# Performance work log

Hardware: AMD Instinct MI355X
Metric: run time of the kernel (lower is better)

## Reference

```python
import jax, jax.numpy as jnp
import numpy as np

IN_FEATURES = 8192
OUT_FEATURES = 28672
BATCH = 8  # tokens; skinny GEMM -> memory-bound weight streaming


def setup_inputs() -> dict:
    key = jax.random.key(0)
    k1, k2, k3, k4 = jax.random.split(key, 4)
    x = jax.random.normal(k1, (BATCH, IN_FEATURES), dtype=jnp.float32)
    # ternary codes in {0,1,2} -> weight values {-1,0,+1}; pack 4 codes / byte
    codes = jax.random.randint(k2, (OUT_FEATURES, IN_FEATURES), 0, 3, dtype=jnp.int32)
    codes4 = codes.reshape(OUT_FEATURES, IN_FEATURES // 4, 4)
    shifts = jnp.array([0, 2, 4, 6], dtype=jnp.int32)
    packed_weight = jnp.sum(codes4 << shifts, axis=-1).astype(jnp.int32)  # [O, I//4]
    weight_scale = jax.random.uniform(k3, (1,), dtype=jnp.float32, minval=0.01, maxval=0.1)
    bias = jax.random.normal(k4, (OUT_FEATURES,), dtype=jnp.float32)
    return {"x": x, "packed_weight": packed_weight, "weight_scale": weight_scale, "bias": bias}


def _unpack_ternary(packed):
    # [O, I//4] int -> [O, I] ternary in {-1,0,1}
    shifts = jnp.array([0, 2, 4, 6], dtype=jnp.int32)
    w = ((packed[:, :, None] >> shifts) & 3) - 1  # [O, I//4, 4]
    return w.reshape(packed.shape[0], -1)


def reference(x, packed_weight, weight_scale, bias):
    B = x.shape[0]
    x_flat = x.reshape(B, IN_FEATURES)
    # per-tensor absmax int8 activation quantization
    absmax = jnp.maximum(jnp.max(jnp.abs(x_flat)), 1e-5)
    act_scale = absmax / 127.0
    x_q = jnp.clip(jnp.round(x_flat / act_scale), -128, 127)  # int8 values, kept f32
    w = _unpack_ternary(packed_weight).astype(jnp.float32)  # [O, I]
    # fused dequant GEMM: integer-valued accumulation, single scalar scale
    acc = jnp.einsum('bi,oi->bo', x_q, w)  # exact in f32 (|acc| << 2^24)
    scale = weight_scale[0] * act_scale
    out = acc * scale + bias
    return out.reshape(B, OUT_FEATURES)
```

## Files before the change

### kernel.cpp

```cpp
#include <hip/hip_runtime.h>
#include <stdint.h>

#define O_FEATS 28672
#define I_FEATS 8192
#define BATCH 8
#define PITCH_W 260

typedef int i32x4 __attribute__((ext_vector_type(4)));


static __device__ __forceinline__ int unpack4(uint32_t p) {
  uint32_t lo = p & 0x0Fu;
  uint32_t hi = (p >> 4) & 0x0Fu;
  uint32_t a = (lo * 0x41u) & 0x0303u;
  uint32_t b = (hi * 0x41u) & 0x0303u;
  return (int)(a | (b << 16));
}

__global__ void k_absmax(const float* __restrict__ x, uint32_t* __restrict__ ws) {
  __shared__ float red[4];
  int t = threadIdx.x;
  float4 v = ((const float4*)x)[blockIdx.x * 256 + t];
  float m = fmaxf(fmaxf(fabsf(v.x), fabsf(v.y)), fmaxf(fabsf(v.z), fabsf(v.w)));
#pragma unroll
  for (int off = 32; off; off >>= 1)
    m = fmaxf(m, __shfl_xor(m, off));
  if ((t & 63) == 0) red[t >> 6] = m;
  __syncthreads();
  if (t == 0)
    ws[16 + blockIdx.x] =
        __float_as_uint(fmaxf(fmaxf(red[0], red[1]), fmaxf(red[2], red[3])));
}

__global__ void k_quant(const float* __restrict__ x, uint32_t* __restrict__ ws) {
  __shared__ float s_amax;
  __shared__ int reds[4];
  int t = threadIdx.x;
  if (blockIdx.x >= 64) {
    int row = 8 + ((blockIdx.x - 64) >> 3), seg = blockIdx.x & 7;
    int k0 = seg * 1024 + t * 4;
    int S = k0 >> 6, g = (k0 >> 4) & 3, j = k0 & 15;
    ws[1024 + ((S * 1024 + (g * 16 + row) * 16 + j) >> 2)] = 0u;
    return;
  }
  int b = blockIdx.x >> 3, seg = blockIdx.x & 7;
  if (t < 64) {
    float m = __uint_as_float(ws[16 + t]);
#pragma unroll
    for (int off = 32; off; off >>= 1)
      m = fmaxf(m, __shfl_xor(m, off));
    if (t == 0) {
      float a = fmaxf(m, 1e-5f);
      s_amax = a;
      ws[0] = __float_as_uint(a);
    }
  }
  __syncthreads();
  float s = s_amax / 127.0f;
  float4 v = ((const float4*)(x + b * I_FEATS + seg * 1024))[t];
  int q0 = (int)fminf(fmaxf(rintf(v.x / s), -128.f), 127.f);
  int q1 = (int)fminf(fmaxf(rintf(v.y / s), -128.f), 127.f);
  int q2 = (int)fminf(fmaxf(rintf(v.z / s), -128.f), 127.f);
  int q3 = (int)fminf(fmaxf(rintf(v.w / s), -128.f), 127.f);
  uint32_t pk = (uint32_t)(q0 & 0xff) | ((uint32_t)(q1 & 0xff) << 8) |
                ((uint32_t)(q2 & 0xff) << 16) | ((uint32_t)(q3 & 0xff) << 24);
  {
    int k0 = seg * 1024 + t * 4;
    int S = k0 >> 6, g = (k0 >> 4) & 3, j = k0 & 15;
    ws[1024 + ((S * 1024 + (g * 16 + b) * 16 + j) >> 2)] = pk;
  }
  int s4 = q0 + q1 + q2 + q3;
#pragma unroll
  for (int off = 32; off; off >>= 1)
    s4 += __shfl_xor(s4, off);
  if ((t & 63) == 0) reds[t >> 6] = s4;
  __syncthreads();
  if (t == 0)
    ws[128 + blockIdx.x] = (uint32_t)(reds[0] + reds[1] + reds[2] + reds[3]);
}

__global__ void __launch_bounds__(256, 4)
k_gemm(const int* __restrict__ Wp, const float* __restrict__ wscale,
       const float* __restrict__ bias, const uint32_t* __restrict__ ws,
       float* __restrict__ out) {
  __shared__ uint32_t Wlds[16 * PITCH_W];
  __shared__ int red[4][32][4];
  __shared__ int s_sumx[BATCH];
  __shared__ float s_scale;

  const int t = threadIdx.x;
  const int wave = t >> 6, lane = t & 63;

  if (t < 64) {
    int p = (int)ws[128 + t];
    p += __shfl_xor(p, 1);
    p += __shfl_xor(p, 2);
    p += __shfl_xor(p, 4);
    if ((t & 7) == 0) s_sumx[t >> 3] = p;
    if (t == 0) s_scale = (__uint_as_float(ws[0]) / 127.0f) * wscale[0];
  }

  const int o_base = blockIdx.x * 16;
  const int m = lane & 15, g = lane >> 4;

  const uint8_t* xqT = (const uint8_t*)(ws + 1024);
  const int4* ap = (const int4*)(xqT + (size_t)(wave * 4) * 1024 + lane * 16);

  const uint8_t* src_base =
      (const uint8_t*)Wp + (size_t)(o_base + wave * 4) * 8192 + lane * 16;
  uint32_t* lds_row0 = &Wlds[(wave * 4) * PITCH_W];

  const uint32_t* bp0 = &Wlds[m * PITCH_W + (wave * 256 + g * 16) / 4];

  i32x4 acc = {0, 0, 0, 0};

  for (int c = 0; c < 8; ++c) {
    __syncthreads();
#pragma unroll
    for (int i = 0; i < 4; ++i) {
      const uint32_t* src = (const uint32_t*)(src_base + (size_t)i * 8192 + c * 1024);
      __builtin_amdgcn_global_load_lds(src, lds_row0 + i * PITCH_W, 16, 0, 0);
    }
    int4 a[4];
#pragma unroll
    for (int s = 0; s < 4; ++s) a[s] = ap[(c * 16 + s) * 64];
    __syncthreads();
#pragma unroll
    for (int s = 0; s < 4; ++s) {
      int4 b = *(const int4*)(bp0 + s * 16);
      i32x4 af, bf;
      af.x = a[s].x; af.y = a[s].y; af.z = a[s].z; af.w = a[s].w;
      bf.x = unpack4((uint32_t)b.x);
      bf.y = unpack4((uint32_t)b.y);
      bf.z = unpack4((uint32_t)b.z);
      bf.w = unpack4((uint32_t)b.w);
      acc = __builtin_amdgcn_mfma_i32_16x16x64_i8(af, bf, acc, 0, 0, 0);
    }
  }

  if (lane < 32) {
#pragma unroll
    for (int r = 0; r < 4; ++r) red[wave][lane][r] = acc[r];
  }
  __syncthreads();

  if (t < 32) {
    const int n = t & 15;
    const int q = t >> 4;
    const int o = o_base + n;
    const float bo = bias[o];
#pragma unroll
    for (int r = 0; r < 4; ++r) {
      int mm = q * 4 + r;
      int tot = red[0][t][r] + red[1][t][r] + red[2][t][r] + red[3][t][r];
      out[mm * O_FEATS + o] = (float)(tot - s_sumx[mm]) * s_scale + bo;
    }
  }
}

extern "C" void kernel_launch(void* const* d_in, const int* in_sizes, int n_in,
                              void* d_out, int out_size, void* d_ws, size_t ws_size,
                              hipStream_t stream) {
  const float* x = (const float*)d_in[0];
  const int* pw = (const int*)d_in[1];
  const float* wscale = (const float*)d_in[2];
  const float* bias = (const float*)d_in[3];
  float* out = (float*)d_out;
  uint32_t* ws = (uint32_t*)d_ws;

  k_absmax<<<64, 256, 0, stream>>>(x, ws);
  k_quant<<<128, 256, 0, stream>>>(x, ws);
  k_gemm<<<O_FEATS / 16, 256, 0, stream>>>(pw, wscale, bias, ws, out);
}
```

Before: 319.6 us.

## Replace LDS weight staging with register double-buffered direct global loads

The GEMM kernel no longer stages weight tiles through shared memory with global_load_lds and two barriers per chunk. Each lane now loads its weight and activation fragments straight from global memory into registers, using two register buffers so the next group's loads are issued before the current group's MFMAs. The K split is also changed so each wave covers one contiguous 2048-byte range instead of interleaved slices. This is meant to remove barrier stalls and LDS round-trips and keep more loads in flight. The trade-off is that each global load instruction now reads only 64 contiguous bytes per row rather than a full contiguous row segment, and the extra buffers use more registers.

```diff
diff --git a/kernel.cpp b/kernel.cpp
--- a/kernel.cpp
+++ b/kernel.cpp
@@ -4,7 +4,6 @@
 #define O_FEATS 28672
 #define I_FEATS 8192
 #define BATCH 8
-#define PITCH_W 260
 
 typedef int i32x4 __attribute__((ext_vector_type(4)));
 
@@ -83,13 +82,19 @@
 k_gemm(const int* __restrict__ Wp, const float* __restrict__ wscale,
        const float* __restrict__ bias, const uint32_t* __restrict__ ws,
        float* __restrict__ out) {
-  __shared__ uint32_t Wlds[16 * PITCH_W];
   __shared__ int red[4][32][4];
   __shared__ int s_sumx[BATCH];
   __shared__ float s_scale;
 
   const int t = threadIdx.x;
   const int wave = t >> 6, lane = t & 63;
+  const int m = lane & 15, g = lane >> 4;
+  const int o_base = blockIdx.x * 16;
+
+  const uint8_t* bsrc = (const uint8_t*)Wp + (size_t)(o_base + m) * 8192 +
+                        wave * 2048 + g * 16;
+  const uint8_t* asrc = (const uint8_t*)(ws + 1024) + (size_t)wave * 32768 +
+                        lane * 16;
 
   if (t < 64) {
     int p = (int)ws[128 + t];
@@ -100,43 +105,57 @@
     if (t == 0) s_scale = (__uint_as_float(ws[0]) / 127.0f) * wscale[0];
   }
 
-  const int o_base = blockIdx.x * 16;
-  const int m = lane & 15, g = lane >> 4;
+  i32x4 acc = {0, 0, 0, 0};
+  int4 bA[4], aA[4], bB[4], aB[4];
 
-  const uint8_t* xqT = (const uint8_t*)(ws + 1024);
-  const int4* ap = (const int4*)(xqT + (size_t)(wave * 4) * 1024 + lane * 16);
+#define LOADG(gi, B, A)                                                   \
+  do {                                                                    \
+    const uint8_t* bp = bsrc + (gi) * 256;                                \
+    const uint8_t* ap = asrc + (gi) * 4096;                               \
+    B[0] = *(const int4*)(bp + 0);                                        \
+    A[0] = *(const int4*)(ap + 0);                                        \
+    B[1] = *(const int4*)(bp + 64);                                       \
+    A[1] = *(const int4*)(ap + 1024);                                     \
+    B[2] = *(const int4*)(bp + 128);                                      \
+    A[2] = *(const int4*)(ap + 2048);                                     \
+    B[3] = *(const int4*)(bp + 192);                                      \
+    A[3] = *(const int4*)(ap + 3072);                                     \
+  } while (0)
 
-  const uint8_t* src_base =
-      (const uint8_t*)Wp + (size_t)(o_base + wave * 4) * 8192 + lane * 16;
-  uint32_t* lds_row0 = &Wlds[(wave * 4) * PITCH_W];
+#define COMPG(B, A)                                                       \
+  do {                                                                    \
+    _Pragma("unroll") for (int s = 0; s < 4; ++s) {                       \
+      i32x4 af, bf;                                                       \
+      af.x = A[s].x;                                                      \
+      af.y = A[s].y;                                                      \
+      af.z = A[s].z;                                                      \
+      af.w = A[s].w;                                                      \
+      bf.x = unpack4((uint32_t)B[s].x);                                   \
+      bf.y = unpack4((uint32_t)B[s].y);                                   \
+      bf.z = unpack4((uint32_t)B[s].z);                                   \
+      bf.w = unpack4((uint32_t)B[s].w);                                   \
+      acc = __builtin_amdgcn_mfma_i32_16x16x64_i8(af, bf, acc, 0, 0, 0);  \
+    }                                                                     \
+  } while (0)
 
-  const uint32_t* bp0 = &Wlds[m * PITCH_W + (wave * 256 + g * 16) / 4];
-
-  i32x4 acc = {0, 0, 0, 0};
-
-  for (int c = 0; c < 8; ++c) {
-    __syncthreads();
-#pragma unroll
-    for (int i = 0; i < 4; ++i) {
-      const uint32_t* src = (const uint32_t*)(src_base + (size_t)i * 8192 + c * 1024);
-      __builtin_amdgcn_global_load_lds(src, lds_row0 + i * PITCH_W, 16, 0, 0);
-    }
-    int4 a[4];
-#pragma unroll
-    for (int s = 0; s < 4; ++s) a[s] = ap[(c * 16 + s) * 64];
-    __syncthreads();
-#pragma unroll
-    for (int s = 0; s < 4; ++s) {
-      int4 b = *(const int4*)(bp0 + s * 16);
-      i32x4 af, bf;
-      af.x = a[s].x; af.y = a[s].y; af.z = a[s].z; af.w = a[s].w;
-      bf.x = unpack4((uint32_t)b.x);
-      bf.y = unpack4((uint32_t)b.y);
-      bf.z = unpack4((uint32_t)b.z);
-      bf.w = unpack4((uint32_t)b.w);
-      acc = __builtin_amdgcn_mfma_i32_16x16x64_i8(af, bf, acc, 0, 0, 0);
-    }
-  }
+  LOADG(0, bA, aA);
+  LOADG(1, bB, aB);
+  COMPG(bA, aA);
+  LOADG(2, bA, aA);
+  COMPG(bB, aB);
+  LOADG(3, bB, aB);
+  COMPG(bA, aA);
+  LOADG(4, bA, aA);
+  COMPG(bB, aB);
+  LOADG(5, bB, aB);
+  COMPG(bA, aA);
+  LOADG(6, bA, aA);
+  COMPG(bB, aB);
+  LOADG(7, bB, aB);
+  COMPG(bA, aA);
+  COMPG(bB, aB);
+#undef LOADG
+#undef COMPG
 
   if (lane < 32) {
 #pragma unroll
```

Measured after the change: 327.6 us. +2.5%, slower.

## Double-buffer weight LDS staging and swizzle LDS layout in ternary GEMM

Applied to the files above, without the earlier changes.

Adds a second LDS buffer for packed weights so the next chunk's global-to-LDS load and activation loads are issued before computing on the current chunk. This replaces the two barriers per iteration with one and overlaps memory latency with the MFMA work. It also XOR-swizzles the source addresses so the LDS reads hit fewer bank conflicts. LDS use per block doubles, which may lower occupancy, and the loop is now fully unrolled.

```diff
diff --git a/kernel.cpp b/kernel.cpp
--- a/kernel.cpp
+++ b/kernel.cpp
@@ -83,13 +83,15 @@
 k_gemm(const int* __restrict__ Wp, const float* __restrict__ wscale,
        const float* __restrict__ bias, const uint32_t* __restrict__ ws,
        float* __restrict__ out) {
-  __shared__ uint32_t Wlds[16 * PITCH_W];
+  __shared__ uint32_t Wlds[2][16 * PITCH_W];
   __shared__ int red[4][32][4];
   __shared__ int s_sumx[BATCH];
   __shared__ float s_scale;
 
   const int t = threadIdx.x;
   const int wave = t >> 6, lane = t & 63;
+  const int m = lane & 15, g = lane >> 4;
+  const int o_base = blockIdx.x * 16;
 
   if (t < 64) {
     int p = (int)ws[128 + t];
@@ -100,43 +102,64 @@
     if (t == 0) s_scale = (__uint_as_float(ws[0]) / 127.0f) * wscale[0];
   }
 
-  const int o_base = blockIdx.x * 16;
-  const int m = lane & 15, g = lane >> 4;
+  const uint8_t* asrc =
+      (const uint8_t*)(ws + 1024) + (size_t)(wave * 4) * 1024 + lane * 16;
 
-  const uint8_t* xqT = (const uint8_t*)(ws + 1024);
-  const int4* ap = (const int4*)(xqT + (size_t)(wave * 4) * 1024 + lane * 16);
+  const uint8_t* wrow_base =
+      (const uint8_t*)Wp + (size_t)(o_base + wave * 4) * 8192;
+  uint32_t* lds_w0 = &Wlds[0][(wave * 4) * PITCH_W];
+  uint32_t* lds_w1 = &Wlds[1][(wave * 4) * PITCH_W];
 
-  const uint8_t* src_base =
-      (const uint8_t*)Wp + (size_t)(o_base + wave * 4) * 8192 + lane * 16;
-  uint32_t* lds_row0 = &Wlds[(wave * 4) * PITCH_W];
+  const int bword = m * PITCH_W + wave * 64 + ((g ^ (m & 3)) << 2);
+  const uint32_t* bp0 = &Wlds[0][bword];
+  const uint32_t* bp1 = &Wlds[1][bword];
 
-  const uint32_t* bp0 = &Wlds[m * PITCH_W + (wave * 256 + g * 16) / 4];
+#define STAGE(c, dst)                                                        \
+  do {                                                                       \
+    _Pragma("unroll") for (int i = 0; i < 4; ++i) {                          \
+      const uint32_t* src = (const uint32_t*)(wrow_base + (size_t)i * 8192 + \
+                                              (c) * 1024 + ((lane ^ i) << 4)); \
+      __builtin_amdgcn_global_load_lds(src, (dst) + i * PITCH_W, 16, 0, 0);  \
+    }                                                                        \
+  } while (0)
 
   i32x4 acc = {0, 0, 0, 0};
+  int4 aA[4], aB[4];
 
+  STAGE(0, lds_w0);
+#pragma unroll
+  for (int s = 0; s < 4; ++s)
+    aA[s] = *(const int4*)(asrc + (size_t)s * 1024);
+  __syncthreads();
+
+#pragma unroll
   for (int c = 0; c < 8; ++c) {
-    __syncthreads();
+    if (c < 7) {
+      STAGE(c + 1, (c & 1) ? lds_w0 : lds_w1);
+      int4* an = (c & 1) ? aA : aB;
 #pragma unroll
-    for (int i = 0; i < 4; ++i) {
-      const uint32_t* src = (const uint32_t*)(src_base + (size_t)i * 8192 + c * 1024);
-      __builtin_amdgcn_global_load_lds(src, lds_row0 + i * PITCH_W, 16, 0, 0);
+      for (int s = 0; s < 4; ++s)
+        an[s] = *(const int4*)(asrc + (size_t)((c + 1) * 16 + s) * 1024);
     }
-    int4 a[4];
-#pragma unroll
-    for (int s = 0; s < 4; ++s) a[s] = ap[(c * 16 + s) * 64];
-    __syncthreads();
+    const uint32_t* bp = (c & 1) ? bp1 : bp0;
+    const int4* A = (c & 1) ? aB : aA;
 #pragma unroll
     for (int s = 0; s < 4; ++s) {
-      int4 b = *(const int4*)(bp0 + s * 16);
+      int4 b = *(const int4*)(bp + s * 16);
       i32x4 af, bf;
-      af.x = a[s].x; af.y = a[s].y; af.z = a[s].z; af.w = a[s].w;
+      af.x = A[s].x;
+      af.y = A[s].y;
+      af.z = A[s].z;
+      af.w = A[s].w;
       bf.x = unpack4((uint32_t)b.x);
       bf.y = unpack4((uint32_t)b.y);
       bf.z = unpack4((uint32_t)b.z);
       bf.w = unpack4((uint32_t)b.w);
       acc = __builtin_amdgcn_mfma_i32_16x16x64_i8(af, bf, acc, 0, 0, 0);
     }
+    __syncthreads();
   }
+#undef STAGE
 
   if (lane < 32) {
 #pragma unroll
```

Result: no change. 320.5 us (+0.3%).
